# Kernel optimization log

Measured on AMD Instinct MI355X. Metric: run time of the kernel, lower is better.

Reference implementation:

```python
import jax, jax.numpy as jnp
import numpy as np

B, S, D, H = 4, 2048, 1024, 16
HD = D // H  # head_size = 64


def setup_inputs() -> dict:
    key = jax.random.key(0)
    kx, kq, kk, kv = jax.random.split(key, 4)
    scale = 1.0 / np.sqrt(D)
    return {
        "x": jax.random.normal(kx, (B, S, D), dtype=jnp.float32),
        "Wq": jax.random.normal(kq, (H, HD, D), dtype=jnp.float32) * scale,
        "Wk": jax.random.normal(kk, (H, HD, D), dtype=jnp.float32) * scale,
        "Wv": jax.random.normal(kv, (H, HD, D), dtype=jnp.float32) * scale,
    }


def reference(x, Wq, Wk, Wv):
    # Per-head projections (Linear with weight [out, in]: y = x @ W.T),
    # vectorized over heads: [B,S,D] x [H,HD,D] -> [B,H,S,HD]
    q = jnp.einsum('bsd,hed->bhse', x, Wq)
    k = jnp.einsum('bsd,hed->bhse', x, Wk)
    v = jnp.einsum('bsd,hed->bhse', x, Wv)

    # Scaled scores: [B,H,S,S]
    att = jnp.einsum('bhqe,bhke->bhqk', q, k) / jnp.sqrt(jnp.asarray(HD, x.dtype))

    # Causal mask (lower-triangular incl. diagonal)
    causal = jnp.tril(jnp.ones((S, S), dtype=bool))
    att = jnp.where(causal, att, -jnp.inf)
    att = jax.nn.softmax(att, axis=-1)

    # Weighted values, then concat heads along feature dim -> [B,S,D]
    out = jnp.einsum('bhqk,bhke->bhqe', att, v)
    out = out.transpose(0, 2, 1, 3).reshape(B, S, H * HD)
    return out
```

## Files before the change

### kernel.cpp

```cpp
#include <hip/hip_runtime.h>
#include <hip/hip_bf16.h>

#define BATCH 4
#define S_LEN 2048
#define D_DIM 1024
#define NHEAD 16
#define HDIM 64

#define QSCALE 0.18033688011112042f

typedef __attribute__((ext_vector_type(8))) __bf16 bf16x8;
typedef __attribute__((ext_vector_type(4))) __bf16 bf16x4;
typedef __attribute__((ext_vector_type(4))) float f32x4;

static __device__ inline unsigned int bf16_bits(float f) {
    __bf16 h = (__bf16)f;
    return (unsigned int)__builtin_bit_cast(unsigned short, h);
}

__global__ __launch_bounds__(256) void cvt_kernel(
    const float* __restrict__ src, __bf16* __restrict__ dst, int n8)
{
    int i = blockIdx.x * 256 + threadIdx.x;
    if (i >= n8) return;
    const f32x4* p = reinterpret_cast<const f32x4*>(src + (size_t)i * 8);
    f32x4 a = p[0], b = p[1];
    bf16x8 r;
    r[0] = (__bf16)a[0]; r[1] = (__bf16)a[1]; r[2] = (__bf16)a[2]; r[3] = (__bf16)a[3];
    r[4] = (__bf16)b[0]; r[5] = (__bf16)b[1]; r[6] = (__bf16)b[2]; r[7] = (__bf16)b[3];
    *reinterpret_cast<bf16x8*>(dst + (size_t)i * 8) = r;
}

__global__ __launch_bounds__(256) void proj_gemm_kernel(
    const __bf16* __restrict__ xb, const __bf16* __restrict__ wb,
    __bf16* __restrict__ qo, __bf16* __restrict__ ko, __bf16* __restrict__ vto)
{
    __shared__ __bf16 As[128][32];
    __shared__ __bf16 Bs[128][32];

    const int tid = threadIdx.x;
    const int l  = tid & 63;
    const int w  = tid >> 6;
    const int wm = w >> 1, wn = w & 1;
    const int lr = l & 15, lg = l >> 4, lk = lg * 8;
    const int m0 = blockIdx.y * 128;
    const int n0 = blockIdx.x * 128;
    const int mat = n0 >> 10;
    const int nb  = n0 & 1023;

    const int sr = l >> 2;
    const int sc = (l & 3) * 8;
    const int g0 = w * 2;

    f32x4 acc[4][4] = {};

    for (int d = 0; d < D_DIM; d += 32) {
        __builtin_amdgcn_global_load_lds(
            (const __attribute__((address_space(1))) void*)(xb + (size_t)(m0 + g0 * 16 + sr) * D_DIM + d + sc),
            (__attribute__((address_space(3))) void*)(&As[g0 * 16][0]), 16, 0, 0);
        __builtin_amdgcn_global_load_lds(
            (const __attribute__((address_space(1))) void*)(xb + (size_t)(m0 + (g0 + 1) * 16 + sr) * D_DIM + d + sc),
            (__attribute__((address_space(3))) void*)(&As[(g0 + 1) * 16][0]), 16, 0, 0);
        __builtin_amdgcn_global_load_lds(
            (const __attribute__((address_space(1))) void*)(wb + (size_t)(n0 + g0 * 16 + sr) * D_DIM + d + sc),
            (__attribute__((address_space(3))) void*)(&Bs[g0 * 16][0]), 16, 0, 0);
        __builtin_amdgcn_global_load_lds(
            (const __attribute__((address_space(1))) void*)(wb + (size_t)(n0 + (g0 + 1) * 16 + sr) * D_DIM + d + sc),
            (__attribute__((address_space(3))) void*)(&Bs[(g0 + 1) * 16][0]), 16, 0, 0);
        __syncthreads();

        bf16x8 af[4], bfr[4];
        #pragma unroll
        for (int mi = 0; mi < 4; ++mi)
            af[mi] = *reinterpret_cast<const bf16x8*>(&As[wm * 64 + mi * 16 + lr][lk]);
        #pragma unroll
        for (int ni = 0; ni < 4; ++ni)
            bfr[ni] = *reinterpret_cast<const bf16x8*>(&Bs[wn * 64 + ni * 16 + lr][lk]);
        #pragma unroll
        for (int mi = 0; mi < 4; ++mi) {
            #pragma unroll
            for (int ni = 0; ni < 4; ++ni)
                acc[mi][ni] = __builtin_amdgcn_mfma_f32_16x16x32_bf16(
                    af[mi], bfr[ni], acc[mi][ni], 0, 0, 0);
        }
        __syncthreads();
    }

    const float oscale = (mat == 0) ? QSCALE : 1.0f;
    #pragma unroll
    for (int mi = 0; mi < 4; ++mi) {
        const int mrow = m0 + wm * 64 + mi * 16 + lg * 4;
        const int b = mrow >> 11;
        const int s = mrow & (S_LEN - 1);
        #pragma unroll
        for (int ni = 0; ni < 4; ++ni) {
            const int n = nb + wn * 64 + ni * 16 + lr;
            const int h = n >> 6;
            const int e = n & 63;
            if (mat == 2) {
                bf16x4 pk;
                #pragma unroll
                for (int r = 0; r < 4; ++r) pk[r] = (__bf16)acc[mi][ni][r];
                *reinterpret_cast<bf16x4*>(
                    vto + ((size_t)(b * NHEAD + h) * HDIM + e) * S_LEN + s) = pk;
            } else {
                __bf16* __restrict__ dst = (mat == 0) ? qo : ko;
                #pragma unroll
                for (int r = 0; r < 4; ++r)
                    dst[((size_t)(b * NHEAD + h) * S_LEN + (s + r)) * HDIM + e] =
                        (__bf16)(acc[mi][ni][r] * oscale);
            }
        }
    }
}

template<bool MASK>
__device__ __attribute__((always_inline)) inline void quad_iter(
    int kv0, int qbase, int lr, int lg, int lk, int swz,
    const __bf16* __restrict__ kp, const __bf16* __restrict__ vp,
    const bf16x8 (&bq0)[4], const bf16x8 (&bq1)[4],
    float (&m_acc)[4], float (&l_acc)[4], f32x4 (&acc)[4][4],
    __bf16* pl_base)
{
    bf16x8 ka0[4], ka1[4];
    #pragma unroll
    for (int c = 0; c < 4; ++c) {
        const __bf16* krow = kp + (size_t)(kv0 + c * 16 + lr) * HDIM;
        ka0[c] = *reinterpret_cast<const bf16x8*>(krow + lk);
        ka1[c] = *reinterpret_cast<const bf16x8*>(krow + 32 + lk);
    }
    bf16x8 av[2][4];
    #pragma unroll
    for (int c2 = 0; c2 < 2; ++c2)
        #pragma unroll
        for (int ni = 0; ni < 4; ++ni)
            av[c2][ni] = *reinterpret_cast<const bf16x8*>(
                vp + (size_t)(ni * 16 + lr) * S_LEN + kv0 + c2 * 32 + lk);

    #pragma unroll
    for (int i = 0; i < 4; ++i) {
        __bf16* pl = pl_base + i * (16 * 64);
        f32x4 s[4];
        __builtin_amdgcn_s_setprio(1);
        #pragma unroll
        for (int c = 0; c < 4; ++c) {
            f32x4 tt = {};
            tt = __builtin_amdgcn_mfma_f32_16x16x32_bf16(ka0[c], bq0[i], tt, 0, 0, 0);
            tt = __builtin_amdgcn_mfma_f32_16x16x32_bf16(ka1[c], bq1[i], tt, 0, 0, 0);
            s[c] = tt;
        }
        __builtin_amdgcn_s_setprio(0);

        if (MASK) {
            const int qrow = qbase + i * 16 + lr;
            #pragma unroll
            for (int c = 0; c < 4; ++c)
                #pragma unroll
                for (int r = 0; r < 4; ++r)
                    if (kv0 + c * 16 + lg * 4 + r > qrow) s[c][r] = -1e30f;
        }

        float a0 = fmaxf(fmaxf(s[0][0], s[0][1]), fmaxf(s[0][2], s[0][3]));
        float a1 = fmaxf(fmaxf(s[1][0], s[1][1]), fmaxf(s[1][2], s[1][3]));
        float a2 = fmaxf(fmaxf(s[2][0], s[2][1]), fmaxf(s[2][2], s[2][3]));
        float a3 = fmaxf(fmaxf(s[3][0], s[3][1]), fmaxf(s[3][2], s[3][3]));
        float mx = fmaxf(fmaxf(a0, a1), fmaxf(a2, a3));
        mx = fmaxf(mx, __shfl_xor(mx, 16));
        mx = fmaxf(mx, __shfl_xor(mx, 32));

        const float mnew = fmaxf(m_acc[i], mx);
        const float sc = exp2f(m_acc[i] - mnew);
        m_acc[i] = mnew;

        float psum = 0.0f;
        #pragma unroll
        for (int c = 0; c < 4; ++c) {
            const float p0 = exp2f(s[c][0] - mnew);
            const float p1 = exp2f(s[c][1] - mnew);
            const float p2 = exp2f(s[c][2] - mnew);
            const float p3 = exp2f(s[c][3] - mnew);
            psum += (p0 + p1) + (p2 + p3);
            uint2 pk;
            pk.x = bf16_bits(p0) | (bf16_bits(p1) << 16);
            pk.y = bf16_bits(p2) | (bf16_bits(p3) << 16);
            *reinterpret_cast<uint2*>(pl + lr * 64 + ((c * 16 + lg * 4) ^ swz)) = pk;
        }
        psum += __shfl_xor(psum, 16);
        psum += __shfl_xor(psum, 32);
        l_acc[i] = l_acc[i] * sc + psum;

        #pragma unroll
        for (int ni = 0; ni < 4; ++ni) acc[i][ni] *= sc;
    }

    __builtin_amdgcn_s_setprio(1);
    #pragma unroll
    for (int c2 = 0; c2 < 2; ++c2) {
        #pragma unroll
        for (int i = 0; i < 4; ++i) {
            __bf16* pl = pl_base + i * (16 * 64);
            const bf16x8 pa = *reinterpret_cast<const bf16x8*>(
                pl + lr * 64 + ((c2 * 32 + lk) ^ swz));
            #pragma unroll
            for (int ni = 0; ni < 4; ++ni)
                acc[i][ni] = __builtin_amdgcn_mfma_f32_16x16x32_bf16(
                    av[c2][ni], pa, acc[i][ni], 0, 0, 0);
        }
    }
    __builtin_amdgcn_s_setprio(0);
}

__global__ __launch_bounds__(64, 2) void attn_kernel(
    const __bf16* __restrict__ q, const __bf16* __restrict__ k,
    const __bf16* __restrict__ vt, float* __restrict__ out)
{
    __shared__ __bf16 plds[4][16][64];

    const int l  = threadIdx.x;
    const int lr = l & 15;
    const int lg = l >> 4;
    const int lk = lg * 8;
    const int swz = (lr & 7) << 3;

    const int n   = blockIdx.x;
    const int xcd = n & 7;
    const int m   = n >> 3;
    const int qq  = 31 - (m >> 3);
    const int bh  = xcd * 8 + (m & 7);

    const __bf16* __restrict__ kp = k  + (size_t)bh * S_LEN * HDIM;
    const __bf16* __restrict__ vp = vt + (size_t)bh * HDIM * S_LEN;
    const int bq = bh >> 4;
    const int hq = bh & 15;

    const int qbase = qq * 64;
    const int iters = qq + 1;

    const __bf16* __restrict__ qp = q + ((size_t)bh * S_LEN + qbase) * HDIM;
    bf16x8 bq0[4], bq1[4];
    #pragma unroll
    for (int i = 0; i < 4; ++i) {
        bq0[i] = *reinterpret_cast<const bf16x8*>(qp + (size_t)(i * 16 + lr) * HDIM + lk);
        bq1[i] = *reinterpret_cast<const bf16x8*>(qp + (size_t)(i * 16 + lr) * HDIM + 32 + lk);
    }

    float m_acc[4], l_acc[4];
    f32x4 acc[4][4] = {};
    #pragma unroll
    for (int i = 0; i < 4; ++i) { m_acc[i] = -1e30f; l_acc[i] = 0.0f; }

    __bf16* pl_base = &plds[0][0][0];

    #pragma unroll 1
    for (int j = 0; j < iters - 1; ++j)
        quad_iter<false>(j * 64, qbase, lr, lg, lk, swz, kp, vp,
                         bq0, bq1, m_acc, l_acc, acc, pl_base);
    quad_iter<true>((iters - 1) * 64, qbase, lr, lg, lk, swz, kp, vp,
                    bq0, bq1, m_acc, l_acc, acc, pl_base);

    #pragma unroll
    for (int i = 0; i < 4; ++i) {
        const float liv = 1.0f / l_acc[i];
        float* orow = out + (size_t)(bq * S_LEN + qbase + i * 16 + lr) * D_DIM + hq * HDIM;
        #pragma unroll
        for (int ni = 0; ni < 4; ++ni) {
            f32x4 ox;
            #pragma unroll
            for (int r = 0; r < 4; ++r) ox[r] = acc[i][ni][r] * liv;
            *reinterpret_cast<f32x4*>(orow + ni * 16 + lg * 4) = ox;
        }
    }
}

extern "C" void kernel_launch(void* const* d_in, const int* in_sizes, int n_in,
                              void* d_out, int out_size, void* d_ws, size_t ws_size,
                              hipStream_t stream)
{
    const float* x  = (const float*)d_in[0];
    const float* Wq = (const float*)d_in[1];
    const float* Wk = (const float*)d_in[2];
    const float* Wv = (const float*)d_in[3];
    float* out = (float*)d_out;

    const size_t x_elems = (size_t)BATCH * S_LEN * D_DIM;
    const size_t w_elems = (size_t)D_DIM * D_DIM;
    __bf16* xb   = (__bf16*)d_out;
    __bf16* wcat = xb + x_elems;

    const size_t per_buf = (size_t)BATCH * NHEAD * S_LEN * HDIM;
    __bf16* qb = (__bf16*)d_ws;
    __bf16* kb = qb + per_buf;
    __bf16* vb = kb + per_buf;

    cvt_kernel<<<(int)(x_elems / 8 / 256), 256, 0, stream>>>(x, xb, (int)(x_elems / 8));
    cvt_kernel<<<(int)(w_elems / 8 / 256), 256, 0, stream>>>(Wq, wcat, (int)(w_elems / 8));
    cvt_kernel<<<(int)(w_elems / 8 / 256), 256, 0, stream>>>(Wk, wcat + w_elems, (int)(w_elems / 8));
    cvt_kernel<<<(int)(w_elems / 8 / 256), 256, 0, stream>>>(Wv, wcat + 2 * w_elems, (int)(w_elems / 8));

    dim3 grid1(3 * D_DIM / 128, (BATCH * S_LEN) / 128);
    proj_gemm_kernel<<<grid1, dim3(256), 0, stream>>>(xb, wcat, qb, kb, vb);

    attn_kernel<<<dim3(2048), dim3(64), 0, stream>>>(qb, kb, vb, out);
}
```

Before: 193.0 us.

## Skip online-softmax rescale unless the running max grows past a threshold

Introduces lazy rescaling in the flash-attention loop. The row max is reduced across lanes and the accumulators rescaled only when some lane's new block max exceeds the stored max by more than 8 (log2 units). The per-row sum is kept per lane and reduced across lanes once, at the end. This removes cross-lane shuffles, exp2 calls and accumulator multiplies from the common path, at the cost of a wave-wide vote per row and probabilities that may exceed 1 by up to 2^8 before bf16 packing.

```diff
diff --git a/kernel.cpp b/kernel.cpp
--- a/kernel.cpp
+++ b/kernel.cpp
@@ -115,11 +115,11 @@
 }
 
 template<bool MASK>
-__device__ __attribute__((always_inline)) inline void quad_iter(
+__device__ __attribute__((always_inline)) inline void quad_compute(
     int kv0, int qbase, int lr, int lg, int lk, int swz,
     const __bf16* __restrict__ kp, const __bf16* __restrict__ vp,
     const bf16x8 (&bq0)[4], const bf16x8 (&bq1)[4],
-    float (&m_acc)[4], float (&l_acc)[4], f32x4 (&acc)[4][4],
+    float (&m_acc)[4], float (&l_lane)[4], f32x4 (&acc)[4][4],
     __bf16* pl_base)
 {
     bf16x8 ka0[4], ka1[4];
@@ -131,11 +131,11 @@
     }
     bf16x8 av[2][4];
     #pragma unroll
-    for (int c2 = 0; c2 < 2; ++c2)
-        #pragma unroll
-        for (int ni = 0; ni < 4; ++ni)
-            av[c2][ni] = *reinterpret_cast<const bf16x8*>(
-                vp + (size_t)(ni * 16 + lr) * S_LEN + kv0 + c2 * 32 + lk);
+    for (int ni = 0; ni < 4; ++ni) {
+        const __bf16* vrow = vp + (size_t)(ni * 16 + lr) * S_LEN + kv0;
+        av[0][ni] = *reinterpret_cast<const bf16x8*>(vrow + lk);
+        av[1][ni] = *reinterpret_cast<const bf16x8*>(vrow + 32 + lk);
+    }
 
     #pragma unroll
     for (int i = 0; i < 4; ++i) {
@@ -165,32 +165,33 @@
         float a2 = fmaxf(fmaxf(s[2][0], s[2][1]), fmaxf(s[2][2], s[2][3]));
         float a3 = fmaxf(fmaxf(s[3][0], s[3][1]), fmaxf(s[3][2], s[3][3]));
         float mx = fmaxf(fmaxf(a0, a1), fmaxf(a2, a3));
-        mx = fmaxf(mx, __shfl_xor(mx, 16));
-        mx = fmaxf(mx, __shfl_xor(mx, 32));
-
-        const float mnew = fmaxf(m_acc[i], mx);
-        const float sc = exp2f(m_acc[i] - mnew);
-        m_acc[i] = mnew;
-
+
+        if (!__all(mx - m_acc[i] <= 8.0f)) {
+            mx = fmaxf(mx, __shfl_xor(mx, 16));
+            mx = fmaxf(mx, __shfl_xor(mx, 32));
+            const float mnew = fmaxf(m_acc[i], mx);
+            const float sc = exp2f(m_acc[i] - mnew);
+            l_lane[i] *= sc;
+            #pragma unroll
+            for (int ni = 0; ni < 4; ++ni) acc[i][ni] *= sc;
+            m_acc[i] = mnew;
+        }
+
+        const float mi_ = m_acc[i];
         float psum = 0.0f;
         #pragma unroll
         for (int c = 0; c < 4; ++c) {
-            const float p0 = exp2f(s[c][0] - mnew);
-            const float p1 = exp2f(s[c][1] - mnew);
-            const float p2 = exp2f(s[c][2] - mnew);
-            const float p3 = exp2f(s[c][3] - mnew);
+            const float p0 = exp2f(s[c][0] - mi_);
+            const float p1 = exp2f(s[c][1] - mi_);
+            const float p2 = exp2f(s[c][2] - mi_);
+            const float p3 = exp2f(s[c][3] - mi_);
             psum += (p0 + p1) + (p2 + p3);
             uint2 pk;
             pk.x = bf16_bits(p0) | (bf16_bits(p1) << 16);
             pk.y = bf16_bits(p2) | (bf16_bits(p3) << 16);
             *reinterpret_cast<uint2*>(pl + lr * 64 + ((c * 16 + lg * 4) ^ swz)) = pk;
         }
-        psum += __shfl_xor(psum, 16);
-        psum += __shfl_xor(psum, 32);
-        l_acc[i] = l_acc[i] * sc + psum;
-
-        #pragma unroll
-        for (int ni = 0; ni < 4; ++ni) acc[i][ni] *= sc;
+        l_lane[i] += psum;
     }
 
     __builtin_amdgcn_s_setprio(1);
@@ -244,23 +245,26 @@
         bq1[i] = *reinterpret_cast<const bf16x8*>(qp + (size_t)(i * 16 + lr) * HDIM + 32 + lk);
     }
 
-    float m_acc[4], l_acc[4];
+    float m_acc[4], l_lane[4];
     f32x4 acc[4][4] = {};
     #pragma unroll
-    for (int i = 0; i < 4; ++i) { m_acc[i] = -1e30f; l_acc[i] = 0.0f; }
+    for (int i = 0; i < 4; ++i) { m_acc[i] = -1e30f; l_lane[i] = 0.0f; }
 
     __bf16* pl_base = &plds[0][0][0];
 
     #pragma unroll 1
     for (int j = 0; j < iters - 1; ++j)
-        quad_iter<false>(j * 64, qbase, lr, lg, lk, swz, kp, vp,
-                         bq0, bq1, m_acc, l_acc, acc, pl_base);
-    quad_iter<true>((iters - 1) * 64, qbase, lr, lg, lk, swz, kp, vp,
-                    bq0, bq1, m_acc, l_acc, acc, pl_base);
+        quad_compute<false>(j * 64, qbase, lr, lg, lk, swz, kp, vp,
+                            bq0, bq1, m_acc, l_lane, acc, pl_base);
+    quad_compute<true>((iters - 1) * 64, qbase, lr, lg, lk, swz, kp, vp,
+                       bq0, bq1, m_acc, l_lane, acc, pl_base);
 
     #pragma unroll
     for (int i = 0; i < 4; ++i) {
-        const float liv = 1.0f / l_acc[i];
+        float lt = l_lane[i];
+        lt += __shfl_xor(lt, 16);
+        lt += __shfl_xor(lt, 32);
+        const float liv = 1.0f / lt;
         float* orow = out + (size_t)(bq * S_LEN + qbase + i * 16 + lr) * D_DIM + hq * HDIM;
         #pragma unroll
         for (int ni = 0; ni < 4; ++ni) {
```

Result: faster. 185.9 us (-3.7%).
